# Performance work log

Hardware: AMD Instinct MI355X
Metric: run time of the kernel (lower is better)

The kernel has to match this reference:

```python
import jax, jax.numpy as jnp
import numpy as np

B_, L_, DM, DS, DC, EX = 4, 2048, 1024, 16, 4, 2
DI = DM * EX

def setup_inputs() -> dict:
    key = jax.random.key(0)
    ks = jax.random.split(key, 8)
    s = lambda i, shape, scale: jax.random.normal(ks[i], shape, jnp.float32) * scale
    return dict(
        x=s(0, (B_, L_, DM), 1.0),
        in_proj_w=s(1, (2 * DI, DM), 0.02),
        conv_weight=s(2, (DI, DC), 0.1),
        conv_bias=jnp.zeros((DI,), jnp.float32),
        A_log=jax.random.uniform(ks[3], (DS,), jnp.float32, -4.0, -1.0),
        D=jnp.ones((DI,), jnp.float32),
        delta_w=s(4, (DS, DI), 0.02),
        delta_b=jnp.ones((DS,), jnp.float32),
        B_w=s(5, (DS, DI), 0.02),
        C_w=s(6, (DS, DI), 0.02),
        out_proj_w=s(7, (DM, DI), 0.02),
    )

def reference(x, in_proj_w, conv_weight, conv_bias, A_log, D, delta_w, delta_b, B_w, C_w, out_proj_w):
    Bb, L, Dm = x.shape
    di, dc = conv_weight.shape
    # 1. input projection and split into ssm / gate branches
    x_inner = x @ in_proj_w.T                       # [B,L,2*di]
    x_ssm, x_gate = x_inner[..., :di], x_inner[..., di:]
    # 2. causal depthwise conv1d + SiLU (kernel size dc, per-channel weights)
    xp = jnp.pad(x_ssm, ((0, 0), (dc - 1, 0), (0, 0)))
    xc = conv_bias + sum(xp[:, k:k + L, :] * conv_weight[:, k] for k in range(dc))
    x_conv = jax.nn.silu(xc)                         # [B,L,di]
    # 3. content-aware discretization
    delta = jax.nn.softplus(x_conv @ delta_w.T + delta_b)  # [B,L,N]
    Bs = x_conv @ B_w.T                              # [B,L,N]
    Cs = x_conv @ C_w.T                              # [B,L,N]
    A = -jnp.exp(A_log)                              # [N]
    xavg = x_conv.mean(axis=-1)                      # [B,L]
    # 4. selective SSM scan over L with state h:[B,N]
    def step(h, inp):
        dt, bt, ct, xa = inp                         # [B,N],[B,N],[B,N],[B]
        h = jnp.exp(dt * A) * h + dt * bt * xa[:, None]
        return h, (h * ct).sum(-1)                   # y_t: [B]
    h0 = jnp.zeros((Bb, A.shape[0]), x.dtype)
    _, ys = jax.lax.scan(
        step, h0,
        (delta.transpose(1, 0, 2), Bs.transpose(1, 0, 2), Cs.transpose(1, 0, 2), xavg.T))
    y_ssm = ys.T[..., None]                          # [B,L,1] (broadcasts over di)
    # 5. gate, skip, output projection
    y_gated = y_ssm * jax.nn.silu(x_gate)
    y_skip = y_gated + x_conv * D
    return y_skip @ out_proj_w.T                     # [B,L,D]
```

## Files before the change

kernel.cpp:

```cpp
#include <hip/hip_runtime.h>
#include <cmath>

#define LL 2048
#define NROW 8192
#define DMODEL 1024
#define DINNER 2048
#define NSTATE 16
#define NSEG 64
#define SEGLEN 32

typedef unsigned short u16;
typedef __attribute__((ext_vector_type(8))) unsigned short u16x8;
typedef __attribute__((ext_vector_type(8))) short short8;
typedef __attribute__((ext_vector_type(4))) float floatx4;
typedef __attribute__((ext_vector_type(16))) float floatx16;

__device__ __forceinline__ float bf2f(u16 h) {
    unsigned u = ((unsigned)h) << 16;
    float f;
    __builtin_memcpy(&f, &u, 4);
    return f;
}
__device__ __forceinline__ u16 f2bf(float f) {
    unsigned u;
    __builtin_memcpy(&u, &f, 4);
    u = u + 0x7fffu + ((u >> 16) & 1u);
    return (u16)(u >> 16);
}
__device__ __forceinline__ float silu_f(float x) { return x / (1.f + __expf(-x)); }

__global__ __launch_bounds__(256) void cvt_multi(
    const float* __restrict__ s0, const float* __restrict__ s1,
    const float* __restrict__ s2, const float* __restrict__ s3,
    const float* __restrict__ s4, const float* __restrict__ s5,
    u16* __restrict__ d0, u16* __restrict__ d1, u16* __restrict__ d2,
    u16* __restrict__ d3, u16* __restrict__ d4, u16* __restrict__ d5) {
    int bid = blockIdx.x;
    const float* s;
    u16* d;
    size_t off;
    if (bid < 4096)      { s = s0; d = d0; off = (size_t)bid * 2048; }
    else if (bid < 6144) { s = s1; d = d1; off = (size_t)(bid - 4096) * 2048; }
    else if (bid < 7168) { s = s2; d = d2; off = (size_t)(bid - 6144) * 2048; }
    else if (bid < 7184) { s = s3; d = d3; off = (size_t)(bid - 7168) * 2048; }
    else if (bid < 7200) { s = s4; d = d4; off = (size_t)(bid - 7184) * 2048; }
    else                 { s = s5; d = d5; off = (size_t)(bid - 7200) * 2048; }
    size_t i = off + (size_t)threadIdx.x * 8;
    float4 a = *(const float4*)&s[i];
    float4 b = *(const float4*)&s[i + 4];
    u16x8 o;
    o[0] = f2bf(a.x); o[1] = f2bf(a.y); o[2] = f2bf(a.z); o[3] = f2bf(a.w);
    o[4] = f2bf(b.x); o[5] = f2bf(b.y); o[6] = f2bf(b.z); o[7] = f2bf(b.w);
    *(u16x8*)&d[i] = o;
}

#define GL_LDS(gp, lp)                                                        \
    __builtin_amdgcn_global_load_lds(                                         \
        (const __attribute__((address_space(1))) void*)(gp),                  \
        (__attribute__((address_space(3))) void*)(lp), 16, 0, 0)
#define BAR() __builtin_amdgcn_s_barrier()
#define LGKM0()                                                               \
    do {                                                                      \
        asm volatile("s_waitcnt lgkmcnt(0)" ::: "memory");                    \
        __builtin_amdgcn_sched_barrier(0);                                    \
    } while (0)
#define VMC4() asm volatile("s_waitcnt vmcnt(4)" ::: "memory")

template <int OUT_BF16>
__global__ __launch_bounds__(512, 2) void gemm_bt_256(
    const u16* __restrict__ A, const u16* __restrict__ B,
    void* __restrict__ Cout, int N, int K) {
    __shared__ u16 sA[2][2][128 * 64];
    __shared__ u16 sB[2][2][128 * 64];
    const int tid = threadIdx.x;
    const int lane = tid & 63;
    const int wave = tid >> 6;
    const int wm = wave >> 2;
    const int wn = wave & 3;
    const int bm = blockIdx.y * 256;
    const int bn = blockIdx.x * 256;

    const int gslot = (lane & 7) ^ ((lane >> 3) & 7);
    const int srowoff = lane >> 3;
    const u16* aG = A + (size_t)(bm + wave * 8 + srowoff) * K + gslot * 8;
    const u16* bG = B + (size_t)(bn + wave * 8 + srowoff) * K + gslot * 8;
    const size_t row64 = (size_t)64 * K;
    const size_t row128 = (size_t)128 * K;

#define STAGE_A(buf, h, kt)                                                   \
    do {                                                                      \
        const u16* g_ = aG + (h) * row128 + (size_t)(kt) * 64;                \
        GL_LDS(g_,         &sA[buf][h][wave * 512]);                          \
        GL_LDS(g_ + row64, &sA[buf][h][(8 + wave) * 512]);                    \
    } while (0)
#define STAGE_B(buf, h, kt)                                                   \
    do {                                                                      \
        const u16* g_ = bG + (h) * row128 + (size_t)(kt) * 64;                \
        GL_LDS(g_,         &sB[buf][h][wave * 512]);                          \
        GL_LDS(g_ + row64, &sB[buf][h][(8 + wave) * 512]);                    \
    } while (0)

    const int fr = lane & 15;
    const int kq = lane >> 4;
    const int st0 = kq ^ (fr & 7);
    const int st1 = (4 + kq) ^ (fr & 7);
    const int aB0 = fr * 64 + st0 * 8;
    const int aB1 = fr * 64 + st1 * 8;
    const int bRow = (wn & 1) * 64 + fr;
    const int bB0 = bRow * 64 + st0 * 8;
    const int bB1 = bRow * 64 + st1 * 8;

    floatx4 acc[8][4];
#pragma unroll
    for (int i = 0; i < 8; ++i)
#pragma unroll
        for (int j = 0; j < 4; ++j) acc[i][j] = (floatx4){0.f, 0.f, 0.f, 0.f};

    short8 af[4][2], bf01[2][2], bf23[2][2];

#define MFMA_PH(mibase, BF, nibase)                                           \
    do {                                                                      \
        _Pragma("unroll")                                                     \
        for (int kh = 0; kh < 2; ++kh)                                        \
            _Pragma("unroll")                                                 \
            for (int mi = 0; mi < 4; ++mi)                                    \
                _Pragma("unroll")                                             \
                for (int ni = 0; ni < 2; ++ni)                                \
                    acc[(mibase) + mi][(nibase) + ni] =                       \
                        __builtin_amdgcn_mfma_f32_16x16x32_bf16(              \
                            af[mi][kh], BF[ni][kh],                           \
                            acc[(mibase) + mi][(nibase) + ni], 0, 0, 0);      \
    } while (0)

    STAGE_A(0, 0, 0);
    STAGE_A(0, 1, 0);
    STAGE_B(0, 0, 0);
    STAGE_B(0, 1, 0);
    STAGE_B(1, 0, 1);
    STAGE_B(1, 1, 1);
    VMC4();
    BAR();

    const int NT = K >> 6;
    for (int t = 0; t < NT; ++t) {
        const int cur = t & 1;
        const int nxt = cur ^ 1;
        const int kA = (t + 1) & (NT - 1);
        const int kB = (t + 2) & (NT - 1);
        const u16* aC = &sA[cur][wm][0];
        const u16* bC = &sB[cur][wn >> 1][0];

#pragma unroll
        for (int mi = 0; mi < 4; ++mi) {
            af[mi][0] = *(const short8*)(aC + aB0 + mi * 16 * 64);
            af[mi][1] = *(const short8*)(aC + aB1 + mi * 16 * 64);
        }
#pragma unroll
        for (int ni = 0; ni < 2; ++ni) {
            bf01[ni][0] = *(const short8*)(bC + bB0 + ni * 16 * 64);
            bf01[ni][1] = *(const short8*)(bC + bB1 + ni * 16 * 64);
        }
        STAGE_A(nxt, 0, kA);
        BAR();
        LGKM0();
        __builtin_amdgcn_s_setprio(1);
        MFMA_PH(0, bf01, 0);
        __builtin_amdgcn_s_setprio(0);
        BAR();

#pragma unroll
        for (int ni = 0; ni < 2; ++ni) {
            bf23[ni][0] = *(const short8*)(bC + bB0 + (32 + ni * 16) * 64);
            bf23[ni][1] = *(const short8*)(bC + bB1 + (32 + ni * 16) * 64);
        }
        STAGE_A(nxt, 1, kA);
        BAR();
        LGKM0();
        __builtin_amdgcn_s_setprio(1);
        MFMA_PH(0, bf23, 2);
        __builtin_amdgcn_s_setprio(0);
        BAR();

#pragma unroll
        for (int mi = 0; mi < 4; ++mi) {
            af[mi][0] = *(const short8*)(aC + aB0 + (64 + mi * 16) * 64);
            af[mi][1] = *(const short8*)(aC + aB1 + (64 + mi * 16) * 64);
        }
        STAGE_B(cur, 0, kB);
        BAR();
        LGKM0();
        __builtin_amdgcn_s_setprio(1);
        MFMA_PH(4, bf01, 0);
        __builtin_amdgcn_s_setprio(0);
        BAR();

        STAGE_B(cur, 1, kB);
        BAR();
        __builtin_amdgcn_s_setprio(1);
        MFMA_PH(4, bf23, 2);
        __builtin_amdgcn_s_setprio(0);
        VMC4();
        BAR();
    }

    const int cc = lane & 15;
    const int rb = (lane >> 4) * 4;
#pragma unroll
    for (int mi = 0; mi < 8; ++mi)
#pragma unroll
        for (int ni = 0; ni < 4; ++ni)
#pragma unroll
            for (int r = 0; r < 4; ++r) {
                int grow = bm + wm * 128 + mi * 16 + rb + r;
                int gcol = bn + wn * 64 + ni * 16 + cc;
                float v = acc[mi][ni][r];
                if (OUT_BF16)
                    ((u16*)Cout)[(size_t)grow * N + gcol] = f2bf(v);
                else
                    ((float*)Cout)[(size_t)grow * N + gcol] = v;
            }
#undef STAGE_A
#undef STAGE_B
#undef MFMA_PH
}

template <int OUT_BF16>
__global__ __launch_bounds__(256) void gemm_bt_mfma(
    const u16* __restrict__ A, const u16* __restrict__ B,
    void* __restrict__ Cout, int N, int K) {
    __shared__ u16 As[128 * 32];
    __shared__ u16 Bs[128 * 32];
    const int tid = threadIdx.x;
    const int lane = tid & 63;
    const int wave = tid >> 6;
    const int bm = blockIdx.y * 128;
    const int bn = blockIdx.x * 128;

    const int kbg = (lane & 3) ^ ((lane >> 3) & 3);
    const int srow = lane >> 2;
    const u16* ag[2];
    const u16* bg[2];
#pragma unroll
    for (int p = 0; p < 2; ++p) {
        int c = wave * 2 + p;
        ag[p] = A + (size_t)(bm + c * 16 + srow) * K + kbg * 8;
        bg[p] = B + (size_t)(bn + c * 16 + srow) * K + kbg * 8;
    }
    const int frow = lane & 31;
    const int khi = lane >> 5;
    const int wr = (wave >> 1) * 64;
    const int wc = (wave & 1) * 64;
    int aoff[2][2], boff[2][2];
#pragma unroll
    for (int mi = 0; mi < 2; ++mi)
#pragma unroll
        for (int kh = 0; kh < 2; ++kh) {
            int rA = wr + mi * 32 + frow;
            int rB = wc + mi * 32 + frow;
            int kb = kh * 2 + khi;
            aoff[mi][kh] = rA * 32 + (kb ^ ((rA >> 1) & 3)) * 8;
            boff[mi][kh] = rB * 32 + (kb ^ ((rB >> 1) & 3)) * 8;
        }
    floatx16 acc[2][2];
#pragma unroll
    for (int i = 0; i < 2; ++i)
#pragma unroll
        for (int j = 0; j < 2; ++j) acc[i][j] = (floatx16)(0.f);

    for (int k0 = 0; k0 < K; k0 += 32) {
        __syncthreads();
#pragma unroll
        for (int p = 0; p < 2; ++p) {
            int c = wave * 2 + p;
            __builtin_amdgcn_global_load_lds(
                (const __attribute__((address_space(1))) void*)ag[p],
                (__attribute__((address_space(3))) void*)&As[c * 512], 16, 0, 0);
            __builtin_amdgcn_global_load_lds(
                (const __attribute__((address_space(1))) void*)bg[p],
                (__attribute__((address_space(3))) void*)&Bs[c * 512], 16, 0, 0);
            ag[p] += 32;
            bg[p] += 32;
        }
        __syncthreads();
        short8 af[2][2], bf[2][2];
#pragma unroll
        for (int mi = 0; mi < 2; ++mi)
#pragma unroll
            for (int kh = 0; kh < 2; ++kh) {
                af[mi][kh] = *(const short8*)&As[aoff[mi][kh]];
                bf[mi][kh] = *(const short8*)&Bs[boff[mi][kh]];
            }
#pragma unroll
        for (int kh = 0; kh < 2; ++kh)
#pragma unroll
            for (int mi = 0; mi < 2; ++mi)
#pragma unroll
                for (int ni = 0; ni < 2; ++ni)
                    acc[mi][ni] = __builtin_amdgcn_mfma_f32_32x32x16_bf16(
                        af[mi][kh], bf[ni][kh], acc[mi][ni], 0, 0, 0);
    }
    const int cc = lane & 31;
    const int rbase = 4 * (lane >> 5);
#pragma unroll
    for (int mi = 0; mi < 2; ++mi)
#pragma unroll
        for (int ni = 0; ni < 2; ++ni)
#pragma unroll
            for (int r = 0; r < 16; ++r) {
                int grow = bm + wr + mi * 32 + (r & 3) + 8 * (r >> 2) + rbase;
                int gcol = bn + wc + ni * 32 + cc;
                float v = acc[mi][ni][r];
                if (OUT_BF16)
                    ((u16*)Cout)[(size_t)grow * N + gcol] = f2bf(v);
                else
                    ((float*)Cout)[(size_t)grow * N + gcol] = v;
            }
}

__global__ __launch_bounds__(256) void conv_silu_avg(
    const u16* __restrict__ xin, const float* __restrict__ cw,
    const float* __restrict__ cb, u16* __restrict__ xconv,
    float* __restrict__ xavg) {
    const int blk = blockIdx.x;
    const int b = blk >> 7;
    const int lc = blk & 127;
    const int row0 = b * LL + lc * 16;
    const int tid = threadIdx.x;
    const int lane = tid & 63, wave = tid >> 6;
    const int d0 = tid * 8;
    float4 cwv[8];
    float cbv[8];
#pragma unroll
    for (int e = 0; e < 8; ++e) cwv[e] = *(const float4*)&cw[(d0 + e) * 4];
#pragma unroll
    for (int e = 0; e < 8; e += 4) {
        float4 c = *(const float4*)&cb[d0 + e];
        cbv[e] = c.x; cbv[e + 1] = c.y; cbv[e + 2] = c.z; cbv[e + 3] = c.w;
    }
    u16x8 w0, w1, w2;
    if (lc == 0) {
        w0 = (u16x8)0; w1 = (u16x8)0; w2 = (u16x8)0;
    } else {
        w0 = *(const u16x8*)&xin[(size_t)(row0 - 3) * (2 * DINNER) + d0];
        w1 = *(const u16x8*)&xin[(size_t)(row0 - 2) * (2 * DINNER) + d0];
        w2 = *(const u16x8*)&xin[(size_t)(row0 - 1) * (2 * DINNER) + d0];
    }
    float sums[16];
#pragma unroll
    for (int t = 0; t < 16; ++t) {
        u16x8 cur = *(const u16x8*)&xin[(size_t)(row0 + t) * (2 * DINNER) + d0];
        float lsum = 0.f;
        u16x8 o;
#pragma unroll
        for (int e = 0; e < 8; ++e) {
            float acc = cbv[e];
            acc += bf2f(w0[e]) * cwv[e].x;
            acc += bf2f(w1[e]) * cwv[e].y;
            acc += bf2f(w2[e]) * cwv[e].z;
            acc += bf2f(cur[e]) * cwv[e].w;
            float s = silu_f(acc);
            lsum += s;
            o[e] = f2bf(s);
        }
        *(u16x8*)&xconv[(size_t)(row0 + t) * DINNER + d0] = o;
        sums[t] = lsum;
        w0 = w1; w1 = w2; w2 = cur;
    }
#pragma unroll
    for (int off = 32; off; off >>= 1)
#pragma unroll
        for (int t = 0; t < 16; ++t) sums[t] += __shfl_down(sums[t], off);
    __shared__ float wred[4][16];
    if (lane == 0) {
#pragma unroll
        for (int t = 0; t < 16; ++t) wred[wave][t] = sums[t];
    }
    __syncthreads();
    if (tid < 16)
        xavg[row0 + tid] = (wred[0][tid] + wred[1][tid] + wred[2][tid] + wred[3][tid]) *
                           (1.f / DINNER);
}

__global__ __launch_bounds__(256) void dbc_direct(
    const u16* __restrict__ xconv, const u16* __restrict__ wcat,
    const float* __restrict__ db, const float* __restrict__ A_log,
    const float* __restrict__ xavg,
    float* __restrict__ a_out, float* __restrict__ u_out, float* __restrict__ c_out) {
    __shared__ float part[4][32][48];
    const int tid = threadIdx.x;
    const int lane = tid & 63;
    const int wave = tid >> 6;
    const int bm = blockIdx.x * 32;
    const int fr = lane & 15;
    const int kq = lane >> 4;
    const int k0 = wave * 512 + kq * 8;

    const u16* ap0 = xconv + (size_t)(bm + fr) * DINNER + k0;
    const u16* ap1 = xconv + (size_t)(bm + 16 + fr) * DINNER + k0;
    const u16* bp0 = wcat + (size_t)(fr) * DINNER + k0;
    const u16* bp1 = wcat + (size_t)(16 + fr) * DINNER + k0;
    const u16* bp2 = wcat + (size_t)(32 + fr) * DINNER + k0;

    floatx4 acc[2][3];
#pragma unroll
    for (int mi = 0; mi < 2; ++mi)
#pragma unroll
        for (int ni = 0; ni < 3; ++ni) acc[mi][ni] = (floatx4){0.f, 0.f, 0.f, 0.f};

#pragma unroll 4
    for (int kk = 0; kk < 16; ++kk) {
        short8 a0 = *(const short8*)ap0;
        short8 a1 = *(const short8*)ap1;
        short8 b0 = *(const short8*)bp0;
        short8 b1 = *(const short8*)bp1;
        short8 b2 = *(const short8*)bp2;
        ap0 += 32; ap1 += 32; bp0 += 32; bp1 += 32; bp2 += 32;
        acc[0][0] = __builtin_amdgcn_mfma_f32_16x16x32_bf16(a0, b0, acc[0][0], 0, 0, 0);
        acc[0][1] = __builtin_amdgcn_mfma_f32_16x16x32_bf16(a0, b1, acc[0][1], 0, 0, 0);
        acc[0][2] = __builtin_amdgcn_mfma_f32_16x16x32_bf16(a0, b2, acc[0][2], 0, 0, 0);
        acc[1][0] = __builtin_amdgcn_mfma_f32_16x16x32_bf16(a1, b0, acc[1][0], 0, 0, 0);
        acc[1][1] = __builtin_amdgcn_mfma_f32_16x16x32_bf16(a1, b1, acc[1][1], 0, 0, 0);
        acc[1][2] = __builtin_amdgcn_mfma_f32_16x16x32_bf16(a1, b2, acc[1][2], 0, 0, 0);
    }
    const int cr = kq * 4;
#pragma unroll
    for (int mi = 0; mi < 2; ++mi)
#pragma unroll
        for (int ni = 0; ni < 3; ++ni)
#pragma unroll
            for (int r = 0; r < 4; ++r)
                part[wave][mi * 16 + cr + r][ni * 16 + fr] = acc[mi][ni][r];
    __syncthreads();
#pragma unroll
    for (int it = tid; it < 512; it += 256) {
        int row = it >> 4;
        int s = it & 15;
        float sd = 0.f, sb = 0.f, sc = 0.f;
#pragma unroll
        for (int w = 0; w < 4; ++w) {
            sd += part[w][row][s];
            sb += part[w][row][s + 16];
            sc += part[w][row][s + 32];
        }
        int grow = bm + row;
        float Aa = -__expf(A_log[s]);
        float pre = sd + db[s];
        float delta = (pre > 20.f) ? pre : log1pf(__expf(pre));
        a_out[grow * NSTATE + s] = __expf(delta * Aa);
        u_out[grow * NSTATE + s] = delta * sb * xavg[grow];
        c_out[grow * NSTATE + s] = sc;
    }
}

__global__ __launch_bounds__(256) void scan_p1(
    const float* __restrict__ a, const float* __restrict__ u,
    float* __restrict__ Pc, float* __restrict__ H0c) {
    int gid = blockIdx.x * 256 + threadIdx.x;
    int s = gid & 15, seg = (gid >> 4) & (NSEG - 1), b = gid >> 10;
    size_t base = (size_t)(b * LL + seg * SEGLEN) * NSTATE + s;
    float P = 1.f, h = 0.f;
#pragma unroll 8
    for (int t = 0; t < SEGLEN; ++t) {
        float av = a[base + (size_t)t * NSTATE];
        float uv = u[base + (size_t)t * NSTATE];
        h = fmaf(av, h, uv);
        P *= av;
    }
    int o = (b * NSEG + seg) * NSTATE + s;
    Pc[o] = P;
    H0c[o] = h;
}

__global__ __launch_bounds__(64) void scan_p2(
    const float* __restrict__ Pc, const float* __restrict__ H0c,
    float* __restrict__ hstart) {
    int lane = threadIdx.x;
    int b = lane >> 4, s = lane & 15;
    float h = 0.f;
#pragma unroll 8
    for (int seg = 0; seg < NSEG; ++seg) {
        int o = (b * NSEG + seg) * NSTATE + s;
        hstart[o] = h;
        h = fmaf(Pc[o], h, H0c[o]);
    }
}

__global__ __launch_bounds__(256) void scan_p3(
    const float* __restrict__ a, const float* __restrict__ u,
    const float* __restrict__ c, const float* __restrict__ hstart,
    float* __restrict__ y) {
    int gid = blockIdx.x * 256 + threadIdx.x;
    int s = gid & 15, seg = (gid >> 4) & (NSEG - 1), b = gid >> 10;
    float h = hstart[(b * NSEG + seg) * NSTATE + s];
    size_t base = (size_t)(b * LL + seg * SEGLEN) * NSTATE + s;
#pragma unroll 8
    for (int t = 0; t < SEGLEN; ++t) {
        float av = a[base + (size_t)t * NSTATE];
        float uv = u[base + (size_t)t * NSTATE];
        float cv = c[base + (size_t)t * NSTATE];
        h = fmaf(av, h, uv);
        float p = h * cv;
        p += __shfl_xor(p, 1);
        p += __shfl_xor(p, 2);
        p += __shfl_xor(p, 4);
        p += __shfl_xor(p, 8);
        if (s == 0) y[b * LL + seg * SEGLEN + t] = p;
    }
}

__global__ __launch_bounds__(256) void gate_skip(
    const u16* __restrict__ xin, const float* __restrict__ y,
    const float* __restrict__ Dv, const u16* __restrict__ xconv,
    u16* __restrict__ yskip) {
    size_t i = ((size_t)blockIdx.x * 256 + threadIdx.x) * 8;
    int row = (int)(i >> 11);
    int d = (int)(i & (DINNER - 1));
    u16x8 g = *(const u16x8*)&xin[(size_t)row * (2 * DINNER) + DINNER + d];
    u16x8 xc = *(const u16x8*)&xconv[i];
    float yv = y[row];
    u16x8 o;
#pragma unroll
    for (int e = 0; e < 8; ++e) {
        float gv = silu_f(bf2f(g[e]));
        float v = yv * gv + bf2f(xc[e]) * Dv[d + e];
        o[e] = f2bf(v);
    }
    *(u16x8*)&yskip[i] = o;
}

extern "C" void kernel_launch(void* const* d_in, const int* in_sizes, int n_in,
                              void* d_out, int out_size, void* d_ws, size_t ws_size,
                              hipStream_t stream) {
    const float* x       = (const float*)d_in[0];
    const float* w_in    = (const float*)d_in[1];
    const float* conv_w  = (const float*)d_in[2];
    const float* conv_b  = (const float*)d_in[3];
    const float* A_log   = (const float*)d_in[4];
    const float* Dv      = (const float*)d_in[5];
    const float* delta_w = (const float*)d_in[6];
    const float* delta_b = (const float*)d_in[7];
    const float* B_w     = (const float*)d_in[8];
    const float* C_w     = (const float*)d_in[9];
    const float* out_w   = (const float*)d_in[10];
    float* out = (float*)d_out;

    u16* xb  = (u16*)d_ws;
    u16* wb  = xb + 8388608;
    u16* owb = wb + 4194304;
    u16* wsb = owb + 2097152;
    u16* xin = wsb + 98304;
    u16* xcv = xin + 33554432;
    u16* ysk = xcv + 16777216;
    float* fb     = (float*)(ysk + 16777216);
    float* abuf   = fb;
    float* ubuf   = abuf + 131072;
    float* cbuf   = ubuf + 131072;
    float* pbuf   = cbuf + 131072;
    float* h0buf  = pbuf + 4096;
    float* hsbuf  = h0buf + 4096;
    float* ybuf   = hsbuf + 4096;
    float* avgbuf = ybuf + 8192;

    cvt_multi<<<7216, 256, 0, stream>>>(x, w_in, out_w, delta_w, B_w, C_w,
                                        xb, wb, owb, wsb, wsb + 32768, wsb + 65536);

    gemm_bt_256<1><<<dim3(16, 32), 512, 0, stream>>>(xb, wb, xin, 2 * DINNER, DMODEL);

    conv_silu_avg<<<512, 256, 0, stream>>>(xin, conv_w, conv_b, xcv, avgbuf);
    dbc_direct<<<256, 256, 0, stream>>>(xcv, wsb, delta_b, A_log, avgbuf,
                                        abuf, ubuf, cbuf);

    scan_p1<<<16, 256, 0, stream>>>(abuf, ubuf, pbuf, h0buf);
    scan_p2<<<1, 64, 0, stream>>>(pbuf, h0buf, hsbuf);
    scan_p3<<<16, 256, 0, stream>>>(abuf, ubuf, cbuf, hsbuf, ybuf);

    gate_skip<<<NROW * DINNER / 8 / 256, 256, 0, stream>>>(xin, ybuf, Dv, xcv, ysk);

    gemm_bt_mfma<0><<<dim3(8, 64), 256, 0, stream>>>(ysk, owb, out, DMODEL, DINNER);
}
```

Before: 317.3 us.

## Restructure input-projection GEMM pipeline with register prefetch, swizzle, and fuse scan kernels

The 256x256 GEMM main loop is rewritten to prefetch the next LDS fragments into double register sets while MFMAs run. It cuts the barriers per k-tile from eight to two and unrolls by two to drop the modulo indexing. Block IDs are remapped with an XCD-aware swizzle for better L2 locality. The three scan kernels are fused into one launch per batch, with the cross-segment carry done in shared memory, removing two launches and global round-trips at the cost of only four blocks.

```diff
diff --git a/kernel.cpp b/kernel.cpp
--- a/kernel.cpp
+++ b/kernel.cpp
@@ -59,66 +59,81 @@
         (const __attribute__((address_space(1))) void*)(gp),                  \
         (__attribute__((address_space(3))) void*)(lp), 16, 0, 0)
 #define BAR() __builtin_amdgcn_s_barrier()
+#define SB0() __builtin_amdgcn_sched_barrier(0)
 #define LGKM0()                                                               \
     do {                                                                      \
         asm volatile("s_waitcnt lgkmcnt(0)" ::: "memory");                    \
         __builtin_amdgcn_sched_barrier(0);                                    \
     } while (0)
 #define VMC4() asm volatile("s_waitcnt vmcnt(4)" ::: "memory")
+#define PRIO1() __builtin_amdgcn_s_setprio(1)
+#define PRIO0() __builtin_amdgcn_s_setprio(0)
 
 template <int OUT_BF16>
 __global__ __launch_bounds__(512, 2) void gemm_bt_256(
     const u16* __restrict__ A, const u16* __restrict__ B,
     void* __restrict__ Cout, int N, int K) {
-    __shared__ u16 sA[2][2][128 * 64];
-    __shared__ u16 sB[2][2][128 * 64];
+    __shared__ u16 sAf[2 * 2 * 128 * 64];
+    __shared__ u16 sBf[2 * 2 * 128 * 64];
     const int tid = threadIdx.x;
     const int lane = tid & 63;
     const int wave = tid >> 6;
     const int wm = wave >> 2;
     const int wn = wave & 3;
-    const int bm = blockIdx.y * 256;
-    const int bn = blockIdx.x * 256;
+
+    const int gx = gridDim.x;
+    const int nwg = gx * gridDim.y;
+    const int cpx = nwg >> 3;
+    int lin = blockIdx.y * gx + blockIdx.x;
+    int swz = (lin & 7) * cpx + (lin >> 3);
+    const int bm = (swz / gx) * 256;
+    const int bn = (swz % gx) * 256;
 
     const int gslot = (lane & 7) ^ ((lane >> 3) & 7);
     const int srowoff = lane >> 3;
-    const u16* aG = A + (size_t)(bm + wave * 8 + srowoff) * K + gslot * 8;
-    const u16* bG = B + (size_t)(bn + wave * 8 + srowoff) * K + gslot * 8;
+    const u16* aStage = A + (size_t)(bm + wave * 8 + srowoff) * K + gslot * 8 + 64;
+    const u16* bStage = B + (size_t)(bn + wave * 8 + srowoff) * K + gslot * 8 + 128;
     const size_t row64 = (size_t)64 * K;
     const size_t row128 = (size_t)128 * K;
 
-#define STAGE_A(buf, h, kt)                                                   \
+#define STAGE_A(BUF, H, PTR)                                                  \
     do {                                                                      \
-        const u16* g_ = aG + (h) * row128 + (size_t)(kt) * 64;                \
-        GL_LDS(g_,         &sA[buf][h][wave * 512]);                          \
-        GL_LDS(g_ + row64, &sA[buf][h][(8 + wave) * 512]);                    \
+        GL_LDS((PTR) + (H) * row128,         &sAf[(BUF) * 16384 + (H) * 8192 + wave * 512]); \
+        GL_LDS((PTR) + (H) * row128 + row64, &sAf[(BUF) * 16384 + (H) * 8192 + (8 + wave) * 512]); \
     } while (0)
-#define STAGE_B(buf, h, kt)                                                   \
+#define STAGE_B(BUF, H, PTR)                                                  \
     do {                                                                      \
-        const u16* g_ = bG + (h) * row128 + (size_t)(kt) * 64;                \
-        GL_LDS(g_,         &sB[buf][h][wave * 512]);                          \
-        GL_LDS(g_ + row64, &sB[buf][h][(8 + wave) * 512]);                    \
+        GL_LDS((PTR) + (H) * row128,         &sBf[(BUF) * 16384 + (H) * 8192 + wave * 512]); \
+        GL_LDS((PTR) + (H) * row128 + row64, &sBf[(BUF) * 16384 + (H) * 8192 + (8 + wave) * 512]); \
     } while (0)
 
     const int fr = lane & 15;
     const int kq = lane >> 4;
     const int st0 = kq ^ (fr & 7);
     const int st1 = (4 + kq) ^ (fr & 7);
-    const int aB0 = fr * 64 + st0 * 8;
-    const int aB1 = fr * 64 + st1 * 8;
+    const int aRd0 = wm * 8192 + fr * 64 + st0 * 8;
+    const int aRd1 = wm * 8192 + fr * 64 + st1 * 8;
     const int bRow = (wn & 1) * 64 + fr;
-    const int bB0 = bRow * 64 + st0 * 8;
-    const int bB1 = bRow * 64 + st1 * 8;
-
-    floatx4 acc[8][4];
-#pragma unroll
-    for (int i = 0; i < 8; ++i)
-#pragma unroll
-        for (int j = 0; j < 4; ++j) acc[i][j] = (floatx4){0.f, 0.f, 0.f, 0.f};
-
-    short8 af[4][2], bf01[2][2], bf23[2][2];
-
-#define MFMA_PH(mibase, BF, nibase)                                           \
+    const int bRd0 = (wn >> 1) * 8192 + bRow * 64 + st0 * 8;
+    const int bRd1 = (wn >> 1) * 8192 + bRow * 64 + st1 * 8;
+
+#define RD_A(dst, BUF, R0)                                                    \
+    do {                                                                      \
+        _Pragma("unroll")                                                     \
+        for (int mi = 0; mi < 4; ++mi) {                                      \
+            dst[mi][0] = *(const short8*)&sAf[(BUF) * 16384 + aRd0 + ((R0) + mi * 16) * 64]; \
+            dst[mi][1] = *(const short8*)&sAf[(BUF) * 16384 + aRd1 + ((R0) + mi * 16) * 64]; \
+        }                                                                     \
+    } while (0)
+#define RD_B(dst, BUF, R0)                                                    \
+    do {                                                                      \
+        _Pragma("unroll")                                                     \
+        for (int ni = 0; ni < 2; ++ni) {                                      \
+            dst[ni][0] = *(const short8*)&sBf[(BUF) * 16384 + bRd0 + ((R0) + ni * 16) * 64]; \
+            dst[ni][1] = *(const short8*)&sBf[(BUF) * 16384 + bRd1 + ((R0) + ni * 16) * 64]; \
+        }                                                                     \
+    } while (0)
+#define MFMA_PH(AF, RB, BF, CB)                                               \
     do {                                                                      \
         _Pragma("unroll")                                                     \
         for (int kh = 0; kh < 2; ++kh)                                        \
@@ -126,82 +141,84 @@
             for (int mi = 0; mi < 4; ++mi)                                    \
                 _Pragma("unroll")                                             \
                 for (int ni = 0; ni < 2; ++ni)                                \
-                    acc[(mibase) + mi][(nibase) + ni] =                       \
+                    acc[(RB) + mi][(CB) + ni] =                               \
                         __builtin_amdgcn_mfma_f32_16x16x32_bf16(              \
-                            af[mi][kh], BF[ni][kh],                           \
-                            acc[(mibase) + mi][(nibase) + ni], 0, 0, 0);      \
+                            AF[mi][kh], BF[ni][kh],                           \
+                            acc[(RB) + mi][(CB) + ni], 0, 0, 0);              \
     } while (0)
 
-    STAGE_A(0, 0, 0);
-    STAGE_A(0, 1, 0);
-    STAGE_B(0, 0, 0);
-    STAGE_B(0, 1, 0);
-    STAGE_B(1, 0, 1);
-    STAGE_B(1, 1, 1);
+    floatx4 acc[8][4];
+#pragma unroll
+    for (int i = 0; i < 8; ++i)
+#pragma unroll
+        for (int j = 0; j < 4; ++j) acc[i][j] = (floatx4){0.f, 0.f, 0.f, 0.f};
+
+    short8 afX[4][2], afY[4][2], bf01[2][2], bf23[2][2];
+
+    {
+        const u16* a0 = aStage - 64;
+        const u16* b0 = bStage - 128;
+        STAGE_A(0, 0, a0);
+        STAGE_A(0, 1, a0);
+        STAGE_B(0, 0, b0);
+        STAGE_B(0, 1, b0);
+        STAGE_B(1, 0, b0 + 64);
+        STAGE_B(1, 1, b0 + 64);
+    }
     VMC4();
     BAR();
+    RD_A(afX, 0, 0);
+    RD_B(bf01, 0, 0);
+    SB0();
+
+#define TILE(CUR, NXT)                                                        \
+                  \
+    LGKM0();                                                                  \
+    PRIO1();                                                                  \
+    MFMA_PH(afX, 0, bf01, 0);                                                 \
+    PRIO0();                                                                  \
+    SB0();                                                                    \
+    RD_B(bf23, CUR, 32);                                                      \
+    STAGE_A(NXT, 0, aStage);                                                  \
+    SB0();                                                                    \
+         \
+    LGKM0();                                                                  \
+    PRIO1();                                                                  \
+    MFMA_PH(afX, 0, bf23, 2);                                                 \
+    PRIO0();                                                                  \
+    SB0();                                                                    \
+    RD_A(afY, CUR, 64);                                                       \
+    STAGE_A(NXT, 1, aStage);                                                  \
+    VMC4();                                                \
+    BAR();                                                                    \
+                 \
+    LGKM0();                                                                  \
+    PRIO1();                                                                  \
+    MFMA_PH(afY, 4, bf01, 0);                                                 \
+    PRIO0();                                                                  \
+    SB0();                                                                    \
+    RD_B(bf01, NXT, 0);                                                       \
+    STAGE_B(CUR, 0, bStage);                                                  \
+    SB0();                                                                    \
+             \
+    PRIO1();                                                                  \
+    MFMA_PH(afY, 4, bf23, 2);                                                 \
+    PRIO0();                                                                  \
+    SB0();                                                                    \
+    STAGE_B(CUR, 1, bStage);                                                  \
+    VMC4();                                                \
+    BAR();                                                                    \
+    RD_A(afX, NXT, 0);                                                        \
+    SB0();                                                                    \
+    aStage += 64;                                                             \
+    bStage += 64;
 
     const int NT = K >> 6;
-    for (int t = 0; t < NT; ++t) {
-        const int cur = t & 1;
-        const int nxt = cur ^ 1;
-        const int kA = (t + 1) & (NT - 1);
-        const int kB = (t + 2) & (NT - 1);
-        const u16* aC = &sA[cur][wm][0];
-        const u16* bC = &sB[cur][wn >> 1][0];
-
-#pragma unroll
-        for (int mi = 0; mi < 4; ++mi) {
-            af[mi][0] = *(const short8*)(aC + aB0 + mi * 16 * 64);
-            af[mi][1] = *(const short8*)(aC + aB1 + mi * 16 * 64);
-        }
-#pragma unroll
-        for (int ni = 0; ni < 2; ++ni) {
-            bf01[ni][0] = *(const short8*)(bC + bB0 + ni * 16 * 64);
-            bf01[ni][1] = *(const short8*)(bC + bB1 + ni * 16 * 64);
-        }
-        STAGE_A(nxt, 0, kA);
-        BAR();
-        LGKM0();
-        __builtin_amdgcn_s_setprio(1);
-        MFMA_PH(0, bf01, 0);
-        __builtin_amdgcn_s_setprio(0);
-        BAR();
-
-#pragma unroll
-        for (int ni = 0; ni < 2; ++ni) {
-            bf23[ni][0] = *(const short8*)(bC + bB0 + (32 + ni * 16) * 64);
-            bf23[ni][1] = *(const short8*)(bC + bB1 + (32 + ni * 16) * 64);
-        }
-        STAGE_A(nxt, 1, kA);
-        BAR();
-        LGKM0();
-        __builtin_amdgcn_s_setprio(1);
-        MFMA_PH(0, bf23, 2);
-        __builtin_amdgcn_s_setprio(0);
-        BAR();
-
-#pragma unroll
-        for (int mi = 0; mi < 4; ++mi) {
-            af[mi][0] = *(const short8*)(aC + aB0 + (64 + mi * 16) * 64);
-            af[mi][1] = *(const short8*)(aC + aB1 + (64 + mi * 16) * 64);
-        }
-        STAGE_B(cur, 0, kB);
-        BAR();
-        LGKM0();
-        __builtin_amdgcn_s_setprio(1);
-        MFMA_PH(4, bf01, 0);
-        __builtin_amdgcn_s_setprio(0);
-        BAR();
-
-        STAGE_B(cur, 1, kB);
-        BAR();
-        __builtin_amdgcn_s_setprio(1);
-        MFMA_PH(4, bf23, 2);
-        __builtin_amdgcn_s_setprio(0);
-        VMC4();
-        BAR();
-    }
+    for (int t = 0; t < NT; t += 2) {
+        TILE(0, 1)
+        TILE(1, 0)
+    }
+#undef TILE
 
     const int cc = lane & 15;
     const int rb = (lane >> 4) * 4;
@@ -221,6 +238,8 @@
             }
 #undef STAGE_A
 #undef STAGE_B
+#undef RD_A
+#undef RD_B
 #undef MFMA_PH
 }
 
@@ -452,11 +471,17 @@
     }
 }
 
-__global__ __launch_bounds__(256) void scan_p1(
+__global__ __launch_bounds__(1024) void scan_fused(
     const float* __restrict__ a, const float* __restrict__ u,
-    float* __restrict__ Pc, float* __restrict__ H0c) {
-    int gid = blockIdx.x * 256 + threadIdx.x;
-    int s = gid & 15, seg = (gid >> 4) & (NSEG - 1), b = gid >> 10;
+    const float* __restrict__ c, float* __restrict__ y) {
+    const int b = blockIdx.x;
+    const int tid = threadIdx.x;
+    const int s = tid & 15;
+    const int seg = tid >> 4;
+    __shared__ float Ps[NSEG][NSTATE];
+    __shared__ float Hs[NSEG][NSTATE];
+    __shared__ float HSs[NSEG][NSTATE];
+
     size_t base = (size_t)(b * LL + seg * SEGLEN) * NSTATE + s;
     float P = 1.f, h = 0.f;
 #pragma unroll 8
@@ -466,40 +491,25 @@
         h = fmaf(av, h, uv);
         P *= av;
     }
-    int o = (b * NSEG + seg) * NSTATE + s;
-    Pc[o] = P;
-    H0c[o] = h;
-}
-
-__global__ __launch_bounds__(64) void scan_p2(
-    const float* __restrict__ Pc, const float* __restrict__ H0c,
-    float* __restrict__ hstart) {
-    int lane = threadIdx.x;
-    int b = lane >> 4, s = lane & 15;
-    float h = 0.f;
-#pragma unroll 8
-    for (int seg = 0; seg < NSEG; ++seg) {
-        int o = (b * NSEG + seg) * NSTATE + s;
-        hstart[o] = h;
-        h = fmaf(Pc[o], h, H0c[o]);
-    }
-}
-
-__global__ __launch_bounds__(256) void scan_p3(
-    const float* __restrict__ a, const float* __restrict__ u,
-    const float* __restrict__ c, const float* __restrict__ hstart,
-    float* __restrict__ y) {
-    int gid = blockIdx.x * 256 + threadIdx.x;
-    int s = gid & 15, seg = (gid >> 4) & (NSEG - 1), b = gid >> 10;
-    float h = hstart[(b * NSEG + seg) * NSTATE + s];
-    size_t base = (size_t)(b * LL + seg * SEGLEN) * NSTATE + s;
+    Ps[seg][s] = P;
+    Hs[seg][s] = h;
+    __syncthreads();
+    if (tid < 16) {
+        float hh = 0.f;
+        for (int g = 0; g < NSEG; ++g) {
+            HSs[g][tid] = hh;
+            hh = fmaf(Ps[g][tid], hh, Hs[g][tid]);
+        }
+    }
+    __syncthreads();
+    float h2 = HSs[seg][s];
 #pragma unroll 8
     for (int t = 0; t < SEGLEN; ++t) {
         float av = a[base + (size_t)t * NSTATE];
         float uv = u[base + (size_t)t * NSTATE];
         float cv = c[base + (size_t)t * NSTATE];
-        h = fmaf(av, h, uv);
-        float p = h * cv;
+        h2 = fmaf(av, h2, uv);
+        float p = h2 * cv;
         p += __shfl_xor(p, 1);
         p += __shfl_xor(p, 2);
         p += __shfl_xor(p, 4);
@@ -555,10 +565,7 @@
     float* abuf   = fb;
     float* ubuf   = abuf + 131072;
     float* cbuf   = ubuf + 131072;
-    float* pbuf   = cbuf + 131072;
-    float* h0buf  = pbuf + 4096;
-    float* hsbuf  = h0buf + 4096;
-    float* ybuf   = hsbuf + 4096;
+    float* ybuf   = cbuf + 131072;
     float* avgbuf = ybuf + 8192;
 
     cvt_multi<<<7216, 256, 0, stream>>>(x, w_in, out_w, delta_w, B_w, C_w,
@@ -570,9 +577,7 @@
     dbc_direct<<<256, 256, 0, stream>>>(xcv, wsb, delta_b, A_log, avgbuf,
                                         abuf, ubuf, cbuf);
 
-    scan_p1<<<16, 256, 0, stream>>>(abuf, ubuf, pbuf, h0buf);
-    scan_p2<<<1, 64, 0, stream>>>(pbuf, h0buf, hsbuf);
-    scan_p3<<<16, 256, 0, stream>>>(abuf, ubuf, cbuf, hsbuf, ybuf);
+    scan_fused<<<4, 1024, 0, stream>>>(abuf, ubuf, cbuf, ybuf);
 
     gate_skip<<<NROW * DINNER / 8 / 256, 256, 0, stream>>>(xin, ybuf, Dv, xcv, ysk);
 
```

After: 302.1 us. 1.05x faster.
